# Kernel tuning notes

Hardware: AMD Instinct MI355X
Metric: run time of the kernel (lower is better)

The kernel has to match this reference:

```python
import jax, jax.numpy as jnp
import numpy as np

B_BOXES = 2          # boxes per cell (b in source)
NUM_CLASSES = 20     # pred channels = B_BOXES*5 + NUM_CLASSES = 30
LAMBDA_COORD = 5.0
LAMBDA_NOOBJ = 0.5


def setup_inputs() -> dict:
    key = jax.random.key(0)
    k1, k2, k3 = jax.random.split(key, 3)
    N, S = 16384, 7
    preds = jax.random.uniform(k1, (N, S, S, B_BOXES * 5 + NUM_CLASSES), dtype=jnp.float32)
    targets = jax.random.uniform(k2, (N, S, S, 5 + NUM_CLASSES), dtype=jnp.float32)
    # channel 0 of target is the object indicator c (checked via c == 1)
    obj = (jax.random.uniform(k3, (N, S, S)) < 0.3).astype(jnp.float32)
    targets = targets.at[..., 0].set(obj)
    return {"preds": preds, "targets": targets}


def reference(preds, targets):
    # preds: [N,S,S,30]; targets: [N,S,S,25]
    N, S1, S2, _ = preds.shape
    bboxes = preds[..., : B_BOXES * 5].reshape(N, S1, S2, B_BOXES, 5)
    obj_scores = bboxes[..., 0]                         # [N,S,S,B]
    idx = jnp.argmax(obj_scores, axis=-1)               # [N,S,S] best box by confidence
    best = jnp.take_along_axis(bboxes, idx[..., None, None], axis=3)[..., 0, :]  # [N,S,S,5]

    c_mask = (targets[..., 0] == 1.0)                   # object present per cell

    box_loss = jnp.sum((best[..., 1:5] - targets[..., 1:5]) ** 2, axis=-1)
    pc_loss = (best[..., 0] - targets[..., 0]) ** 2
    class_loss = jnp.sum((preds[..., B_BOXES * 5:] - targets[..., 5:]) ** 2, axis=-1)

    obj_term = LAMBDA_COORD * box_loss + pc_loss + class_loss
    noobj_term = LAMBDA_NOOBJ * jnp.sum(obj_scores ** 2, axis=-1)

    loss = jnp.sum(jnp.where(c_mask, obj_term, noobj_term))
    return loss
```

## Files before the change

kernel.cpp:

```cpp
#include <hip/hip_runtime.h>

#define LAMBDA_COORD 5.0f
#define LAMBDA_NOOBJ 0.5f


typedef float f4u __attribute__((ext_vector_type(4), aligned(4)));
typedef float f2u __attribute__((ext_vector_type(2), aligned(4)));

__global__ void zero_out_kernel(float* out, int n) {
    int i = blockIdx.x * blockDim.x + threadIdx.x;
    if (i < n) out[i] = 0.0f;
}

__global__ __launch_bounds__(256, 6) void yolo_loss_kernel(
    const float* __restrict__ preds, const float* __restrict__ targets,
    float* __restrict__ out, int n_cells)
{
    __shared__ float s_part[4];
    const int tid = threadIdx.x;
    const int c = blockIdx.x * 256 + tid;

    float loss = 0.0f;
    if (c < n_cells) {
        const float* pbase = preds + (size_t)c * 30;
        const float* tbase = targets + (size_t)c * 25;
        const f4u* pp = (const f4u*)pbase;
        const f4u* tp = (const f4u*)tbase;

        f4u P0 = pp[0], P1 = pp[1], P2 = pp[2], P3 = pp[3];
        f4u P4 = pp[4], P5 = pp[5], P6 = pp[6];
        f2u P7 = *(const f2u*)(pbase + 28);
        f4u T0 = tp[0], T1 = tp[1], T2 = tp[2], T3 = tp[3];
        f4u T4 = tp[4], T5 = tp[5];
        float t24 = tbase[24];

        float p0 = P0.x, p5c = P1.y;
        bool pick1 = p5c > p0;
        float b0 = pick1 ? p5c  : p0;
        float b1 = pick1 ? P1.z : P0.y;
        float b2 = pick1 ? P1.w : P0.z;
        float b3 = pick1 ? P2.x : P0.w;
        float b4 = pick1 ? P2.y : P1.x;

        float t0 = T0.x;
        float d1 = b1 - T0.y, d2 = b2 - T0.z, d3 = b3 - T0.w, d4 = b4 - T1.x;
        float box_loss = d1 * d1 + d2 * d2 + d3 * d3 + d4 * d4;
        float dpc = b0 - t0;
        float pc_loss = dpc * dpc;

        float cl = 0.0f, d;
        d = P2.z - T1.y; cl += d * d;
        d = P2.w - T1.z; cl += d * d;
        d = P3.x - T1.w; cl += d * d;
        d = P3.y - T2.x; cl += d * d;
        d = P3.z - T2.y; cl += d * d;
        d = P3.w - T2.z; cl += d * d;
        d = P4.x - T2.w; cl += d * d;
        d = P4.y - T3.x; cl += d * d;
        d = P4.z - T3.y; cl += d * d;
        d = P4.w - T3.z; cl += d * d;
        d = P5.x - T3.w; cl += d * d;
        d = P5.y - T4.x; cl += d * d;
        d = P5.z - T4.y; cl += d * d;
        d = P5.w - T4.z; cl += d * d;
        d = P6.x - T4.w; cl += d * d;
        d = P6.y - T5.x; cl += d * d;
        d = P6.z - T5.y; cl += d * d;
        d = P6.w - T5.z; cl += d * d;
        d = P7.x - T5.w; cl += d * d;
        d = P7.y - t24;  cl += d * d;

        float obj_term = LAMBDA_COORD * box_loss + pc_loss + cl;
        float noobj_term = LAMBDA_NOOBJ * (p0 * p0 + p5c * p5c);
        loss = (t0 == 1.0f) ? obj_term : noobj_term;
    }

    #pragma unroll
    for (int off = 32; off > 0; off >>= 1)
        loss += __shfl_down(loss, off, 64);

    const int wave = tid >> 6;
    if ((tid & 63) == 0) s_part[wave] = loss;
    __syncthreads();
    if (tid == 0) {
        float s = s_part[0] + s_part[1] + s_part[2] + s_part[3];
        atomicAdd(out, s);
    }
}

extern "C" void kernel_launch(void* const* d_in, const int* in_sizes, int n_in,
                              void* d_out, int out_size, void* d_ws, size_t ws_size,
                              hipStream_t stream) {
    const float* preds   = (const float*)d_in[0];
    const float* targets = (const float*)d_in[1];
    float* out = (float*)d_out;

    const int n_cells = in_sizes[0] / 30;

    zero_out_kernel<<<(out_size + 255) / 256, 256, 0, stream>>>(out, out_size);

    const int grid = (n_cells + 255) / 256;
    yolo_loss_kernel<<<grid, 256, 0, stream>>>(preds, targets, out, n_cells);
}
```

Measured before the change: 193.6 us.

## Process four cells per thread with software-pipelined register prefetch

Each thread now handles four cells spaced a quarter of the array apart. It loads the next cell's preds and targets into registers before computing the loss of the current one, so memory loads overlap with arithmetic. The grid shrinks fourfold, which also cuts per-block reductions and atomics, and launch bounds drop to 2 blocks per CU to allow more registers. It assumes n_cells is divisible by 4, since any leftover cells are silently dropped, and it lowers occupancy for a kernel that is bandwidth bound.

After: 214.5 us. 1.11x slower.

```diff
diff --git a/kernel.cpp b/kernel.cpp
--- a/kernel.cpp
+++ b/kernel.cpp
@@ -7,80 +7,100 @@
 typedef float f4u __attribute__((ext_vector_type(4), aligned(4)));
 typedef float f2u __attribute__((ext_vector_type(2), aligned(4)));
 
+struct Cell {
+    f4u P0, P1, P2, P3, P4, P5, P6; f2u P7;
+    f4u T0, T1, T2, T3, T4, T5; float t24;
+};
+
+__device__ __forceinline__ Cell load_cell(const float* __restrict__ p,
+                                          const float* __restrict__ t) {
+    Cell c;
+    const f4u* p4 = (const f4u*)p;
+    const f4u* t4 = (const f4u*)t;
+    c.P0 = p4[0]; c.P1 = p4[1]; c.P2 = p4[2]; c.P3 = p4[3];
+    c.P4 = p4[4]; c.P5 = p4[5]; c.P6 = p4[6];
+    c.P7 = *(const f2u*)(p + 28);
+    c.T0 = t4[0]; c.T1 = t4[1]; c.T2 = t4[2]; c.T3 = t4[3];
+    c.T4 = t4[4]; c.T5 = t4[5];
+    c.t24 = t[24];
+    return c;
+}
+
+__device__ __forceinline__ float cell_loss(const Cell& c) {
+    float p0 = c.P0.x, p5c = c.P1.y;
+    bool pick1 = p5c > p0;
+    float b0 = pick1 ? p5c    : p0;
+    float b1 = pick1 ? c.P1.z : c.P0.y;
+    float b2 = pick1 ? c.P1.w : c.P0.z;
+    float b3 = pick1 ? c.P2.x : c.P0.w;
+    float b4 = pick1 ? c.P2.y : c.P1.x;
+
+    float t0 = c.T0.x;
+    float d1 = b1 - c.T0.y, d2 = b2 - c.T0.z, d3 = b3 - c.T0.w, d4 = b4 - c.T1.x;
+    float box_loss = d1 * d1 + d2 * d2 + d3 * d3 + d4 * d4;
+    float dpc = b0 - t0;
+    float pc_loss = dpc * dpc;
+
+    float cl = 0.0f, d;
+    d = c.P2.z - c.T1.y; cl += d * d;
+    d = c.P2.w - c.T1.z; cl += d * d;
+    d = c.P3.x - c.T1.w; cl += d * d;
+    d = c.P3.y - c.T2.x; cl += d * d;
+    d = c.P3.z - c.T2.y; cl += d * d;
+    d = c.P3.w - c.T2.z; cl += d * d;
+    d = c.P4.x - c.T2.w; cl += d * d;
+    d = c.P4.y - c.T3.x; cl += d * d;
+    d = c.P4.z - c.T3.y; cl += d * d;
+    d = c.P4.w - c.T3.z; cl += d * d;
+    d = c.P5.x - c.T3.w; cl += d * d;
+    d = c.P5.y - c.T4.x; cl += d * d;
+    d = c.P5.z - c.T4.y; cl += d * d;
+    d = c.P5.w - c.T4.z; cl += d * d;
+    d = c.P6.x - c.T4.w; cl += d * d;
+    d = c.P6.y - c.T5.x; cl += d * d;
+    d = c.P6.z - c.T5.y; cl += d * d;
+    d = c.P6.w - c.T5.z; cl += d * d;
+    d = c.P7.x - c.T5.w; cl += d * d;
+    d = c.P7.y - c.t24;  cl += d * d;
+
+    float obj_term = LAMBDA_COORD * box_loss + pc_loss + cl;
+    float noobj_term = LAMBDA_NOOBJ * (p0 * p0 + p5c * p5c);
+    return (t0 == 1.0f) ? obj_term : noobj_term;
+}
+
 __global__ void zero_out_kernel(float* out, int n) {
     int i = blockIdx.x * blockDim.x + threadIdx.x;
     if (i < n) out[i] = 0.0f;
 }
 
-__global__ __launch_bounds__(256, 6) void yolo_loss_kernel(
+__global__ __launch_bounds__(256, 2) void yolo_loss_kernel(
     const float* __restrict__ preds, const float* __restrict__ targets,
     float* __restrict__ out, int n_cells)
 {
     __shared__ float s_part[4];
     const int tid = threadIdx.x;
+    const int q = n_cells >> 2;
     const int c = blockIdx.x * 256 + tid;
 
-    float loss = 0.0f;
-    if (c < n_cells) {
-        const float* pbase = preds + (size_t)c * 30;
-        const float* tbase = targets + (size_t)c * 25;
-        const f4u* pp = (const f4u*)pbase;
-        const f4u* tp = (const f4u*)tbase;
-
-        f4u P0 = pp[0], P1 = pp[1], P2 = pp[2], P3 = pp[3];
-        f4u P4 = pp[4], P5 = pp[5], P6 = pp[6];
-        f2u P7 = *(const f2u*)(pbase + 28);
-        f4u T0 = tp[0], T1 = tp[1], T2 = tp[2], T3 = tp[3];
-        f4u T4 = tp[4], T5 = tp[5];
-        float t24 = tbase[24];
-
-        float p0 = P0.x, p5c = P1.y;
-        bool pick1 = p5c > p0;
-        float b0 = pick1 ? p5c  : p0;
-        float b1 = pick1 ? P1.z : P0.y;
-        float b2 = pick1 ? P1.w : P0.z;
-        float b3 = pick1 ? P2.x : P0.w;
-        float b4 = pick1 ? P2.y : P1.x;
-
-        float t0 = T0.x;
-        float d1 = b1 - T0.y, d2 = b2 - T0.z, d3 = b3 - T0.w, d4 = b4 - T1.x;
-        float box_loss = d1 * d1 + d2 * d2 + d3 * d3 + d4 * d4;
-        float dpc = b0 - t0;
-        float pc_loss = dpc * dpc;
-
-        float cl = 0.0f, d;
-        d = P2.z - T1.y; cl += d * d;
-        d = P2.w - T1.z; cl += d * d;
-        d = P3.x - T1.w; cl += d * d;
-        d = P3.y - T2.x; cl += d * d;
-        d = P3.z - T2.y; cl += d * d;
-        d = P3.w - T2.z; cl += d * d;
-        d = P4.x - T2.w; cl += d * d;
-        d = P4.y - T3.x; cl += d * d;
-        d = P4.z - T3.y; cl += d * d;
-        d = P4.w - T3.z; cl += d * d;
-        d = P5.x - T3.w; cl += d * d;
-        d = P5.y - T4.x; cl += d * d;
-        d = P5.z - T4.y; cl += d * d;
-        d = P5.w - T4.z; cl += d * d;
-        d = P6.x - T4.w; cl += d * d;
-        d = P6.y - T5.x; cl += d * d;
-        d = P6.z - T5.y; cl += d * d;
-        d = P6.w - T5.z; cl += d * d;
-        d = P7.x - T5.w; cl += d * d;
-        d = P7.y - t24;  cl += d * d;
-
-        float obj_term = LAMBDA_COORD * box_loss + pc_loss + cl;
-        float noobj_term = LAMBDA_NOOBJ * (p0 * p0 + p5c * p5c);
-        loss = (t0 == 1.0f) ? obj_term : noobj_term;
+    float acc = 0.0f;
+    if (c < q) {
+        Cell A = load_cell(preds + (size_t)c * 30, targets + (size_t)c * 25);
+        #pragma unroll
+        for (int i = 1; i < 4; ++i) {
+            const size_t cc = (size_t)(c + i * q);
+            Cell B = load_cell(preds + cc * 30, targets + cc * 25);
+            acc += cell_loss(A);
+            A = B;
+        }
+        acc += cell_loss(A);
     }
 
     #pragma unroll
     for (int off = 32; off > 0; off >>= 1)
-        loss += __shfl_down(loss, off, 64);
+        acc += __shfl_down(acc, off, 64);
 
     const int wave = tid >> 6;
-    if ((tid & 63) == 0) s_part[wave] = loss;
+    if ((tid & 63) == 0) s_part[wave] = acc;
     __syncthreads();
     if (tid == 0) {
         float s = s_part[0] + s_part[1] + s_part[2] + s_part[3];
@@ -99,6 +119,6 @@
 
     zero_out_kernel<<<(out_size + 255) / 256, 256, 0, stream>>>(out, out_size);
 
-    const int grid = (n_cells + 255) / 256;
+    const int grid = (n_cells / 4 + 255) / 256;
     yolo_loss_kernel<<<grid, 256, 0, stream>>>(preds, targets, out, n_cells);
 }
```
